# Kernel tuning notes

Hardware: AMD Instinct MI355X
Metric: run time of the kernel (lower is better)

## Reference

```python
import jax, jax.numpy as jnp
import numpy as np

NEG_CAUSAL = -1e10  # matches torch buffer triu(ones*-1e10, diag=1)
NEG_PAD = -10000.0
NUM_HEADS = 16


def setup_inputs() -> dict:
    key = jax.random.key(0)
    ks = jax.random.split(key, 6)
    B, S, D = 2, 2048, 1024
    scale = 0.02
    return {
        "hidden_states": jax.random.normal(ks[0], (B, S, D), jnp.float32),
        "attention_mask": jnp.ones((B, S), jnp.float32),
        "Wq": jax.random.normal(ks[1], (D, D), jnp.float32) * scale,
        "bq": jnp.zeros((D,), jnp.float32),
        "Wk": jax.random.normal(ks[2], (D, D), jnp.float32) * scale,
        "bk": jnp.zeros((D,), jnp.float32),
        "Wv": jax.random.normal(ks[3], (D, D), jnp.float32) * scale,
        "bv": jnp.zeros((D,), jnp.float32),
        "Wo": jax.random.normal(ks[4], (D, D), jnp.float32) * scale,
        "bo": jnp.zeros((D,), jnp.float32),
    }


def reference(hidden_states, attention_mask, Wq, bq, Wk, bk, Wv, bv, Wo, bo):
    B, S, D = hidden_states.shape
    H = NUM_HEADS
    hd = D // H

    def heads(x):  # [B,S,D] -> [B,H,S,hd]
        return x.reshape(B, S, H, hd).transpose(0, 2, 1, 3)

    q = heads(hidden_states @ Wq + bq)
    k = heads(hidden_states @ Wk + bk)
    v = heads(hidden_states @ Wv + bv)

    scores = jnp.einsum("bhqd,bhkd->bhqk", q, k) / jnp.sqrt(jnp.float32(hd))
    causal = jnp.triu(jnp.full((S, S), NEG_CAUSAL, jnp.float32), k=1)
    scores = scores + causal
    # additive padding mask: (1 - m) * -10000, broadcast over heads and query pos
    scores = scores + (1.0 - attention_mask)[:, None, None, :] * NEG_PAD

    probs = jax.nn.softmax(scores, axis=-1)
    # dropout p=0.1 is inactive in eval mode (training=False)
    ctx = jnp.einsum("bhqk,bhkd->bhqd", probs, v)
    ctx = ctx.transpose(0, 2, 1, 3).reshape(B, S, D)
    return ctx @ Wo + bo
```

## Files before the change

### kernel.cpp

```cpp
#include <hip/hip_runtime.h>

typedef __attribute__((ext_vector_type(8))) short short8_t;
typedef __attribute__((ext_vector_type(4))) float float4_t;
typedef unsigned short u16;
typedef unsigned int u32;
typedef unsigned long long u64;

__device__ inline u16 f2bf(float x) {
  union { float f; u32 u; } v; v.f = x;
  u32 r = v.u + 0x7FFFu + ((v.u >> 16) & 1u);
  return (u16)(r >> 16);
}
#if __has_builtin(__builtin_amdgcn_cvt_pk_bf16_f32)
typedef __attribute__((ext_vector_type(2))) __bf16 bf162_t;
__device__ inline u32 pk2(float a, float b) {
  union { bf162_t v; u32 u; } cv;
  cv.v = __builtin_amdgcn_cvt_pk_bf16_f32(a, b);
  return cv.u;
}
#else
__device__ inline u32 pk2(float a, float b) {
  return (u32)f2bf(a) | ((u32)f2bf(b) << 16);
}
#endif

__global__ __launch_bounds__(256) void prologue(const float* __restrict__ X,
                                                const float* __restrict__ Wq, const float* __restrict__ Wk,
                                                const float* __restrict__ Wv, const float* __restrict__ Wo,
                                                u16* __restrict__ Xb, u16* __restrict__ WqkvT,
                                                u16* __restrict__ WoT, const float* __restrict__ maskp,
                                                u32* __restrict__ flags) {
  __shared__ float tls[32][33];
  int bid = blockIdx.x;
  if (bid < 4096) {
    int i = bid * 256 + threadIdx.x;
    float4_t x = ((const float4_t*)X)[i];
    union { u32 u[2]; u64 ll; } o;
    o.u[0] = pk2(x[0], x[1]);
    o.u[1] = pk2(x[2], x[3]);
    ((u64*)Xb)[i] = o.ll;
  } else if (bid < 8192) {
    int t = bid - 4096;
    int mat = t >> 10, tile = t & 1023;
    const float* W = (mat == 0) ? Wq : (mat == 1) ? Wk : (mat == 2) ? Wv : Wo;
    u16* WT = (mat < 3) ? WqkvT + ((size_t)mat << 20) : WoT;
    int tx = threadIdx.x & 31, ty = threadIdx.x >> 5;
    int c0 = (tile & 31) * 32, r0 = (tile >> 5) * 32;
    #pragma unroll
    for (int i = 0; i < 4; ++i)
      tls[ty + i * 8][tx] = W[(r0 + ty + i * 8) * 1024 + c0 + tx];
    __syncthreads();
    #pragma unroll
    for (int i = 0; i < 4; ++i)
      WT[(size_t)(c0 + ty + i * 8) * 1024 + r0 + tx] = f2bf(tls[tx][ty + i * 8]);
  } else {
    int b = bid - 8192;
    const float* mb = maskp + (b << 11) + threadIdx.x * 8;
    bool ok = true;
    #pragma unroll
    for (int i = 0; i < 8; ++i) ok &= (mb[i] == 1.0f);
    u64 bal = __ballot(ok);
    int w = threadIdx.x >> 6;
    if ((threadIdx.x & 63) == 0) tls[0][w] = (bal == ~0ull) ? 1.0f : 0.0f;
    __syncthreads();
    if (threadIdx.x == 0)
      flags[b] = (tls[0][0] != 0.0f && tls[0][1] != 0.0f &&
                  tls[0][2] != 0.0f && tls[0][3] != 0.0f) ? 1u : 0u;
  }
}

__global__ __launch_bounds__(256) void gemm128(const u16* __restrict__ A, const u16* __restrict__ BT,
                                               const float* __restrict__ bias0, const float* __restrict__ bias1,
                                               const float* __restrict__ bias2,
                                               void* __restrict__ o0, void* __restrict__ o1, void* __restrict__ o2,
                                               int mode) {
  __shared__ __align__(16) u16 Als[128 * 64];
  __shared__ __align__(16) u16 Bls[128 * 64];
  int g = blockIdx.x, m0t, n0t;
  if (mode == 4) {
    int mh = g / 384, r = g - mh * 384;
    n0t = r >> 4;
    m0t = mh * 16 + (r & 15);
  } else {
    m0t = g & 31;
    n0t = g >> 5;
  }
  const int m0 = m0t * 128, n0 = n0t * 128;
  const int lane = threadIdx.x & 63, wave = threadIdx.x >> 6;
  const int quad = lane >> 4, c = lane & 15;
  const int wm = wave >> 1, wn = wave & 1;

  const int srow = lane >> 3, schunk = lane & 7;
  int soff[4], dst[4];
  #pragma unroll
  for (int q = 0; q < 4; ++q) {
    int r = wave * 32 + q * 8 + srow;
    soff[q] = r * 1024 + (schunk << 3);
    dst[q]  = r * 64 + ((schunk ^ (r & 7)) << 3);
  }
  const u16* gA = A + (size_t)m0 * 1024;
  const u16* gB = BT + (size_t)n0 * 1024;

  int ar[2][4], br[2][4];
  #pragma unroll
  for (int ko = 0; ko < 2; ++ko) {
    #pragma unroll
    for (int i = 0; i < 4; ++i) {
      int rowa = wm * 64 + i * 16 + c;
      ar[ko][i] = rowa * 64 + (((ko * 4 + quad) ^ (rowa & 7)) << 3);
      int rowb = wn * 64 + i * 16 + c;
      br[ko][i] = rowb * 64 + (((ko * 4 + quad) ^ (rowb & 7)) << 3);
    }
  }

  short8_t ra[4], rb[4];
  #pragma unroll
  for (int q = 0; q < 4; ++q) ra[q] = *(const short8_t*)(gA + soff[q]);
  #pragma unroll
  for (int q = 0; q < 4; ++q) rb[q] = *(const short8_t*)(gB + soff[q]);

  float4_t acc[4][4] = {};
  for (int k0 = 0; k0 < 1024; k0 += 64) {
    #pragma unroll
    for (int q = 0; q < 4; ++q) *(short8_t*)&Als[dst[q]] = ra[q];
    #pragma unroll
    for (int q = 0; q < 4; ++q) *(short8_t*)&Bls[dst[q]] = rb[q];
    __syncthreads();
    if (k0 < 960) {
      #pragma unroll
      for (int q = 0; q < 4; ++q) ra[q] = *(const short8_t*)(gA + soff[q] + k0 + 64);
      #pragma unroll
      for (int q = 0; q < 4; ++q) rb[q] = *(const short8_t*)(gB + soff[q] + k0 + 64);
    }
    #pragma unroll
    for (int ko = 0; ko < 2; ++ko) {
      short8_t af[4], bfr[4];
      #pragma unroll
      for (int i = 0; i < 4; ++i) af[i] = *(const short8_t*)&Als[ar[ko][i]];
      #pragma unroll
      for (int j = 0; j < 4; ++j) bfr[j] = *(const short8_t*)&Bls[br[ko][j]];
      #pragma unroll
      for (int i = 0; i < 4; ++i)
        #pragma unroll
        for (int j = 0; j < 4; ++j)
          acc[i][j] = __builtin_amdgcn_mfma_f32_16x16x32_bf16(af[i], bfr[j], acc[i][j], 0, 0, 0);
    }
    __syncthreads();
  }

  const int mrow = m0 + wm * 64, ncol = n0 + wn * 64;
  if (mode == 3) {
    float* o = (float*)o0;
    #pragma unroll
    for (int i = 0; i < 4; ++i) {
      #pragma unroll
      for (int j = 0; j < 4; ++j) {
        int colb = ncol + j * 16 + c;
        float bv = bias0[colb];
        int rowb = mrow + i * 16 + quad * 4;
        #pragma unroll
        for (int r = 0; r < 4; ++r)
          o[(size_t)(rowb + r) * 1024 + colb] = acc[i][j][r] + bv;
      }
    }
  } else {
    #pragma unroll
    for (int j = 0; j < 4; ++j) {
      int colb = ncol + j * 16 + c;
      int which = colb >> 10;
      int n1 = colb & 1023, h = n1 >> 6, d = n1 & 63;
      const float* bp = (which == 0) ? bias0 : (which == 1 ? bias1 : bias2);
      float bv = bp[n1];
      #pragma unroll
      for (int i = 0; i < 4; ++i) {
        int rowb = mrow + i * 16 + quad * 4;
        int b = rowb >> 11, s = rowb & 2047;
        if (which == 2) {
          u16* o = (u16*)o2 + (((size_t)(b * 16 + h) * 64 + d) * 2048 + s);
          union { u32 u[2]; u64 ll; } ov;
          ov.u[0] = pk2(acc[i][j][0] + bv, acc[i][j][1] + bv);
          ov.u[1] = pk2(acc[i][j][2] + bv, acc[i][j][3] + bv);
          *(u64*)o = ov.ll;
        } else {
          float sc = (which == 0) ? 0.18033688011112042f : 1.0f;
          u16* o = (u16*)((which == 0) ? o0 : o1);
          #pragma unroll
          for (int r = 0; r < 4; ++r)
            o[(((size_t)(b * 16 + h) * 2048 + (s + r)) << 6) + d] = f2bf((acc[i][j][r] + bv) * sc);
        }
      }
    }
  }
}

__device__ inline short8_t p_to_b_swap(const float* p) {
  u32 a0 = pk2(p[0], p[1]), a1 = pk2(p[2], p[3]);
  u32 b0 = pk2(p[4], p[5]), b1 = pk2(p[6], p[7]);
  asm("v_permlane32_swap_b32 %0, %1" : "+v"(a0), "+v"(b0));
  asm("v_permlane32_swap_b32 %0, %1" : "+v"(a1), "+v"(b1));
  asm("v_permlane16_swap_b32 %0, %1" : "+v"(a0), "+v"(b0));
  asm("v_permlane16_swap_b32 %0, %1" : "+v"(a1), "+v"(b1));
  union { u32 u[4]; short8_t v; } pf;
  pf.u[0] = a0; pf.u[1] = a1; pf.u[2] = b0; pf.u[3] = b1;
  return pf.v;
}

__global__ __launch_bounds__(256, 4) void attn_kernel(const u16* __restrict__ Q, const u16* __restrict__ K,
                                                      const u16* __restrict__ VT, const float* __restrict__ mask,
                                                      const u32* __restrict__ flags, u16* __restrict__ ctx) {
  __shared__ __align__(16) u16 Kls[2 * 64 * 64];
  __shared__ __align__(16) u16 Vls[2 * 64 * 64];
  const float C1 = 10000.0f * 1.4426950408889634f;
  int w = threadIdx.x >> 6, lane = threadIdx.x & 63;
  int quad = lane >> 4, c = lane & 15;
  int g = blockIdx.x;
  int bh = (g & 7) * 4 + ((g >> 3) & 3);
  int u = g >> 5;
  int qt = (u < 16) ? (31 - u) : (u - 16);
  int b = bh >> 4, h = bh & 15;
  bool ones = flags && (flags[b] != 0);
  const u16* Kp = K + ((size_t)bh << 17);
  const u16* Vp = VT + ((size_t)bh << 17);
  const float* mp = mask + (b << 11);
  int q0 = qt * 64 + w * 16;

  const u16* Qp = Q + (((size_t)bh * 2048 + q0 + c) << 6) + quad * 8;
  short8_t qf0 = *(const short8_t*)(Qp);
  short8_t qf1 = *(const short8_t*)(Qp + 32);

  const int srow = lane >> 3, schunk = lane & 7;
  const u16* gK[2]; const u16* gV[2]; int dK[2], dV[2];
  #pragma unroll
  for (int i = 0; i < 2; ++i) {
    int R = w * 16 + i * 8 + srow;
    gK[i] = Kp + R * 64 + (schunk << 3);
    dK[i] = R * 64 + ((schunk ^ (R & 7)) << 3);
    gV[i] = Vp + (size_t)R * 2048 + (schunk << 3);
    dV[i] = R * 64 + ((schunk ^ (R & 7)) << 3);
  }

  int koff[4][2];
  #pragma unroll
  for (int kg = 0; kg < 4; ++kg) {
    int r = kg * 16 + c;
    #pragma unroll
    for (int ko = 0; ko < 2; ++ko)
      koff[kg][ko] = r * 64 + (((ko * 4 + quad) ^ (r & 7)) << 3);
  }
  int voff[4][2];
  #pragma unroll
  for (int dblk = 0; dblk < 4; ++dblk) {
    int d = dblk * 16 + c;
    #pragma unroll
    for (int kc = 0; kc < 2; ++kc)
      voff[dblk][kc] = d * 64 + (((kc * 4 + quad) ^ (d & 7)) << 3);
  }

  int ke[8];
  #pragma unroll
  for (int e = 0; e < 8; ++e) ke[e] = ((e >> 2) << 4) + quad * 4 + (e & 3);
  int thr = w * 16 + c;

  float4_t O[4] = {};
  float l = 0.0f;

  short8_t kreg[2], vreg[2];
  #pragma unroll
  for (int i = 0; i < 2; ++i) { kreg[i] = *(const short8_t*)(gK[i]); vreg[i] = *(const short8_t*)(gV[i]); }

  for (int t = 0; t <= qt; ++t) {
    int kb = t << 6;
    int bufo = (t & 1) << 12;
    #pragma unroll
    for (int i = 0; i < 2; ++i) *(short8_t*)&Kls[bufo + dK[i]] = kreg[i];
    #pragma unroll
    for (int i = 0; i < 2; ++i) *(short8_t*)&Vls[bufo + dV[i]] = vreg[i];
    __syncthreads();
    short8_t vf[4][2];
    #pragma unroll
    for (int dblk = 0; dblk < 4; ++dblk)
      #pragma unroll
      for (int kc = 0; kc < 2; ++kc)
        vf[dblk][kc] = *(const short8_t*)&Vls[bufo + voff[dblk][kc]];
    if (t < qt) {
      int kb2 = (t + 1) << 6;
      #pragma unroll
      for (int i = 0; i < 2; ++i) {
        kreg[i] = *(const short8_t*)(gK[i] + (size_t)kb2 * 64);
        vreg[i] = *(const short8_t*)(gV[i] + kb2);
      }
    }
    float4_t s[4];
    __builtin_amdgcn_s_setprio(1);
    #pragma unroll
    for (int kg = 0; kg < 4; ++kg) {
      short8_t k0 = *(const short8_t*)&Kls[bufo + koff[kg][0]];
      short8_t k1 = *(const short8_t*)&Kls[bufo + koff[kg][1]];
      float4_t a = {};
      a = __builtin_amdgcn_mfma_f32_16x16x32_bf16(k0, qf0, a, 0, 0, 0);
      a = __builtin_amdgcn_mfma_f32_16x16x32_bf16(k1, qf1, a, 0, 0, 0);
      s[kg] = a;
    }
    __builtin_amdgcn_s_setprio(0);
    float4_t mpl[4];
    if (!ones) {
      #pragma unroll
      for (int kg = 0; kg < 4; ++kg)
        mpl[kg] = (*(const float4_t*)(mp + kb + kg * 16 + quad * 4) - 1.0f) * C1;
    }
    bool diag = (t == qt);
    short8_t pf[2];
    #pragma unroll
    for (int kc = 0; kc < 2; ++kc) {
      float p[8];
      #pragma unroll
      for (int e = 0; e < 8; ++e) {
        int kg = kc * 2 + (e >> 2);
        p[e] = s[kg][e & 3];
        if (!ones) p[e] += mpl[kg][e & 3];
      }
      if (diag) {
        #pragma unroll
        for (int e = 0; e < 8; ++e) {
          int ko2 = kc * 32 + ke[e];
          p[e] = (ko2 > thr) ? -50.0f : p[e];
        }
      }
      #pragma unroll
      for (int e = 0; e < 8; ++e) p[e] = exp2f(p[e]);
      float t01 = p[0] + p[1], t23 = p[2] + p[3];
      float t45 = p[4] + p[5], t67 = p[6] + p[7];
      l += (t01 + t23) + (t45 + t67);
      pf[kc] = p_to_b_swap(p);
    }
    __builtin_amdgcn_s_setprio(1);
    #pragma unroll
    for (int dblk = 0; dblk < 4; ++dblk) {
      O[dblk] = __builtin_amdgcn_mfma_f32_16x16x32_bf16(vf[dblk][0], pf[0], O[dblk], 0, 0, 0);
      O[dblk] = __builtin_amdgcn_mfma_f32_16x16x32_bf16(vf[dblk][1], pf[1], O[dblk], 0, 0, 0);
    }
    __builtin_amdgcn_s_setprio(0);
  }
  l += __shfl_xor(l, 16);
  l += __shfl_xor(l, 32);
  float rl = 1.0f / l;
  u16* op = ctx + ((size_t)(b * 2048 + q0 + c) * 1024 + h * 64 + quad * 4);
  #pragma unroll
  for (int dblk = 0; dblk < 4; ++dblk) {
    union { u32 uu[2]; u64 ll; } ov;
    ov.uu[0] = pk2(O[dblk][0] * rl, O[dblk][1] * rl);
    ov.uu[1] = pk2(O[dblk][2] * rl, O[dblk][3] * rl);
    *(u64*)(op + dblk * 16) = ov.ll;
  }
}

extern "C" void kernel_launch(void* const* d_in, const int* in_sizes, int n_in,
                              void* d_out, int out_size, void* d_ws, size_t ws_size,
                              hipStream_t stream) {
  const float* X    = (const float*)d_in[0];
  const float* mask = (const float*)d_in[1];
  const float* Wq   = (const float*)d_in[2];
  const float* bq   = (const float*)d_in[3];
  const float* Wk   = (const float*)d_in[4];
  const float* bk   = (const float*)d_in[5];
  const float* Wv   = (const float*)d_in[6];
  const float* bv   = (const float*)d_in[7];
  const float* Wo   = (const float*)d_in[8];
  const float* bo   = (const float*)d_in[9];

  char* w = (char*)d_ws;
  u16* Xb     = (u16*)(w);
  u16* WqkvT  = (u16*)(w + (8ull  << 20));
  u16* WoT    = (u16*)(w + (14ull << 20));
  u16* Qb     = (u16*)(w + (16ull << 20));
  u16* Kb     = (u16*)(w + (24ull << 20));
  u16* VTb    = (u16*)(w + (32ull << 20));
  u16* Ctx    = (u16*)(w + (40ull << 20));
  u32* flags  = (ws_size >= (48ull << 20) + 8) ? (u32*)(w + (48ull << 20)) : nullptr;

  prologue<<<flags ? 8194 : 8192, 256, 0, stream>>>(X, Wq, Wk, Wv, Wo, Xb, WqkvT, WoT, mask, flags);
  gemm128<<<768, 256, 0, stream>>>(Xb, WqkvT, bq, bk, bv, Qb, Kb, VTb, 4);
  attn_kernel<<<1024, 256, 0, stream>>>(Qb, Kb, VTb, mask, flags, Ctx);
  gemm128<<<256, 256, 0, stream>>>(Ctx, WoT, bo, bo, bo, d_out, d_out, d_out, 3);
}
```

Before: 207.5 us.

## Process 128-query tiles per block with two query groups per wave

Each attention block now covers 128 queries (32 per wave, as two 16-row groups), so each K/V tile loaded into shared memory serves twice as many queries and the grid halves to 512 blocks. Row sums are now computed with extra MFMAs against a ones vector instead of scalar adds plus cross-lane shuffles, and V fragments are read from LDS right before use. Causal skipping becomes per-wave (waves skip tiles beyond their rows). The cost is more registers (launch bounds lowered to 2), fewer blocks for load balance, and extra MFMA work for the row sums.

After: 195.4 us. 5.8% less time.

```diff
diff --git a/kernel.cpp b/kernel.cpp
--- a/kernel.cpp
+++ b/kernel.cpp
@@ -205,7 +205,31 @@
   return pf.v;
 }
 
-__global__ __launch_bounds__(256, 4) void attn_kernel(const u16* __restrict__ Q, const u16* __restrict__ K,
+__device__ inline void softmax_half(const float4_t* s, const float4_t* mpl, bool ones,
+                                    bool diag, int thr, int kb, const int* ke, short8_t* pf) {
+  #pragma unroll
+  for (int kc = 0; kc < 2; ++kc) {
+    float p[8];
+    #pragma unroll
+    for (int e = 0; e < 8; ++e) {
+      int kg = kc * 2 + (e >> 2);
+      p[e] = s[kg][e & 3];
+      if (!ones) p[e] += mpl[kg][e & 3];
+    }
+    if (diag) {
+      #pragma unroll
+      for (int e = 0; e < 8; ++e) {
+        int keyg = kb + kc * 32 + ke[e];
+        p[e] = (keyg > thr) ? -50.0f : p[e];
+      }
+    }
+    #pragma unroll
+    for (int e = 0; e < 8; ++e) p[e] = exp2f(p[e]);
+    pf[kc] = p_to_b_swap(p);
+  }
+}
+
+__global__ __launch_bounds__(256, 2) void attn_kernel(const u16* __restrict__ Q, const u16* __restrict__ K,
                                                       const u16* __restrict__ VT, const float* __restrict__ mask,
                                                       const u32* __restrict__ flags, u16* __restrict__ ctx) {
   __shared__ __align__(16) u16 Kls[2 * 64 * 64];
@@ -216,17 +240,20 @@
   int g = blockIdx.x;
   int bh = (g & 7) * 4 + ((g >> 3) & 3);
   int u = g >> 5;
-  int qt = (u < 16) ? (31 - u) : (u - 16);
+  int qt = (u < 8) ? (15 - u) : (u - 8);
   int b = bh >> 4, h = bh & 15;
   bool ones = flags && (flags[b] != 0);
   const u16* Kp = K + ((size_t)bh << 17);
   const u16* Vp = VT + ((size_t)bh << 17);
   const float* mp = mask + (b << 11);
-  int q0 = qt * 64 + w * 16;
+  int q0 = qt * 128 + w * 32;
+  int nt = 2 * qt + 2;
 
   const u16* Qp = Q + (((size_t)bh * 2048 + q0 + c) << 6) + quad * 8;
-  short8_t qf0 = *(const short8_t*)(Qp);
-  short8_t qf1 = *(const short8_t*)(Qp + 32);
+  short8_t qa0 = *(const short8_t*)(Qp);
+  short8_t qa1 = *(const short8_t*)(Qp + 32);
+  short8_t qb0 = *(const short8_t*)(Qp + (16 << 6));
+  short8_t qb1 = *(const short8_t*)(Qp + (16 << 6) + 32);
 
   const int srow = lane >> 3, schunk = lane & 7;
   const u16* gK[2]; const u16* gV[2]; int dK[2], dV[2];
@@ -259,16 +286,19 @@
   int ke[8];
   #pragma unroll
   for (int e = 0; e < 8; ++e) ke[e] = ((e >> 2) << 4) + quad * 4 + (e & 3);
-  int thr = w * 16 + c;
-
-  float4_t O[4] = {};
-  float l = 0.0f;
+  int thrA = q0 + c;
+  int thrB = q0 + 16 + c;
+  union { u32 uu[4]; short8_t v; } onesf;
+  onesf.uu[0] = onesf.uu[1] = onesf.uu[2] = onesf.uu[3] = 0x3F803F80u;
+
+  float4_t OA[4] = {}, OB[4] = {};
+  float4_t lA = {}, lB = {};
 
   short8_t kreg[2], vreg[2];
   #pragma unroll
   for (int i = 0; i < 2; ++i) { kreg[i] = *(const short8_t*)(gK[i]); vreg[i] = *(const short8_t*)(gV[i]); }
 
-  for (int t = 0; t <= qt; ++t) {
+  for (int t = 0; t < nt; ++t) {
     int kb = t << 6;
     int bufo = (t & 1) << 12;
     #pragma unroll
@@ -276,13 +306,7 @@
     #pragma unroll
     for (int i = 0; i < 2; ++i) *(short8_t*)&Vls[bufo + dV[i]] = vreg[i];
     __syncthreads();
-    short8_t vf[4][2];
-    #pragma unroll
-    for (int dblk = 0; dblk < 4; ++dblk)
-      #pragma unroll
-      for (int kc = 0; kc < 2; ++kc)
-        vf[dblk][kc] = *(const short8_t*)&Vls[bufo + voff[dblk][kc]];
-    if (t < qt) {
+    if (t < nt - 1) {
       int kb2 = (t + 1) << 6;
       #pragma unroll
       for (int i = 0; i < 2; ++i) {
@@ -290,16 +314,22 @@
         vreg[i] = *(const short8_t*)(gV[i] + kb2);
       }
     }
-    float4_t s[4];
+    if (kb > q0 + 31) continue;
+
+    float4_t sA[4], sB[4];
     __builtin_amdgcn_s_setprio(1);
     #pragma unroll
     for (int kg = 0; kg < 4; ++kg) {
       short8_t k0 = *(const short8_t*)&Kls[bufo + koff[kg][0]];
       short8_t k1 = *(const short8_t*)&Kls[bufo + koff[kg][1]];
       float4_t a = {};
-      a = __builtin_amdgcn_mfma_f32_16x16x32_bf16(k0, qf0, a, 0, 0, 0);
-      a = __builtin_amdgcn_mfma_f32_16x16x32_bf16(k1, qf1, a, 0, 0, 0);
-      s[kg] = a;
+      a = __builtin_amdgcn_mfma_f32_16x16x32_bf16(k0, qa0, a, 0, 0, 0);
+      a = __builtin_amdgcn_mfma_f32_16x16x32_bf16(k1, qa1, a, 0, 0, 0);
+      sA[kg] = a;
+      float4_t bb = {};
+      bb = __builtin_amdgcn_mfma_f32_16x16x32_bf16(k0, qb0, bb, 0, 0, 0);
+      bb = __builtin_amdgcn_mfma_f32_16x16x32_bf16(k1, qb1, bb, 0, 0, 0);
+      sB[kg] = bb;
     }
     __builtin_amdgcn_s_setprio(0);
     float4_t mpl[4];
@@ -308,49 +338,43 @@
       for (int kg = 0; kg < 4; ++kg)
         mpl[kg] = (*(const float4_t*)(mp + kb + kg * 16 + quad * 4) - 1.0f) * C1;
     }
-    bool diag = (t == qt);
-    short8_t pf[2];
-    #pragma unroll
-    for (int kc = 0; kc < 2; ++kc) {
-      float p[8];
-      #pragma unroll
-      for (int e = 0; e < 8; ++e) {
-        int kg = kc * 2 + (e >> 2);
-        p[e] = s[kg][e & 3];
-        if (!ones) p[e] += mpl[kg][e & 3];
-      }
-      if (diag) {
-        #pragma unroll
-        for (int e = 0; e < 8; ++e) {
-          int ko2 = kc * 32 + ke[e];
-          p[e] = (ko2 > thr) ? -50.0f : p[e];
-        }
-      }
-      #pragma unroll
-      for (int e = 0; e < 8; ++e) p[e] = exp2f(p[e]);
-      float t01 = p[0] + p[1], t23 = p[2] + p[3];
-      float t45 = p[4] + p[5], t67 = p[6] + p[7];
-      l += (t01 + t23) + (t45 + t67);
-      pf[kc] = p_to_b_swap(p);
-    }
+    bool diag = (kb + 63 > q0);
+    short8_t pfA[2], pfB[2];
+    softmax_half(sA, mpl, ones, diag, thrA, kb, ke, pfA);
+    softmax_half(sB, mpl, ones, diag, thrB, kb, ke, pfB);
     __builtin_amdgcn_s_setprio(1);
     #pragma unroll
     for (int dblk = 0; dblk < 4; ++dblk) {
-      O[dblk] = __builtin_amdgcn_mfma_f32_16x16x32_bf16(vf[dblk][0], pf[0], O[dblk], 0, 0, 0);
-      O[dblk] = __builtin_amdgcn_mfma_f32_16x16x32_bf16(vf[dblk][1], pf[1], O[dblk], 0, 0, 0);
-    }
+      short8_t vf0 = *(const short8_t*)&Vls[bufo + voff[dblk][0]];
+      short8_t vf1 = *(const short8_t*)&Vls[bufo + voff[dblk][1]];
+      OA[dblk] = __builtin_amdgcn_mfma_f32_16x16x32_bf16(vf0, pfA[0], OA[dblk], 0, 0, 0);
+      OA[dblk] = __builtin_amdgcn_mfma_f32_16x16x32_bf16(vf1, pfA[1], OA[dblk], 0, 0, 0);
+      OB[dblk] = __builtin_amdgcn_mfma_f32_16x16x32_bf16(vf0, pfB[0], OB[dblk], 0, 0, 0);
+      OB[dblk] = __builtin_amdgcn_mfma_f32_16x16x32_bf16(vf1, pfB[1], OB[dblk], 0, 0, 0);
+    }
+    lA = __builtin_amdgcn_mfma_f32_16x16x32_bf16(onesf.v, pfA[0], lA, 0, 0, 0);
+    lA = __builtin_amdgcn_mfma_f32_16x16x32_bf16(onesf.v, pfA[1], lA, 0, 0, 0);
+    lB = __builtin_amdgcn_mfma_f32_16x16x32_bf16(onesf.v, pfB[0], lB, 0, 0, 0);
+    lB = __builtin_amdgcn_mfma_f32_16x16x32_bf16(onesf.v, pfB[1], lB, 0, 0, 0);
     __builtin_amdgcn_s_setprio(0);
   }
-  l += __shfl_xor(l, 16);
-  l += __shfl_xor(l, 32);
-  float rl = 1.0f / l;
-  u16* op = ctx + ((size_t)(b * 2048 + q0 + c) * 1024 + h * 64 + quad * 4);
+  float rlA = 1.0f / lA[0];
+  u16* opA = ctx + ((size_t)(b * 2048 + q0 + c) * 1024 + h * 64 + quad * 4);
   #pragma unroll
   for (int dblk = 0; dblk < 4; ++dblk) {
     union { u32 uu[2]; u64 ll; } ov;
-    ov.uu[0] = pk2(O[dblk][0] * rl, O[dblk][1] * rl);
-    ov.uu[1] = pk2(O[dblk][2] * rl, O[dblk][3] * rl);
-    *(u64*)(op + dblk * 16) = ov.ll;
+    ov.uu[0] = pk2(OA[dblk][0] * rlA, OA[dblk][1] * rlA);
+    ov.uu[1] = pk2(OA[dblk][2] * rlA, OA[dblk][3] * rlA);
+    *(u64*)(opA + dblk * 16) = ov.ll;
+  }
+  float rlB = 1.0f / lB[0];
+  u16* opB = ctx + ((size_t)(b * 2048 + q0 + 16 + c) * 1024 + h * 64 + quad * 4);
+  #pragma unroll
+  for (int dblk = 0; dblk < 4; ++dblk) {
+    union { u32 uu[2]; u64 ll; } ov;
+    ov.uu[0] = pk2(OB[dblk][0] * rlB, OB[dblk][1] * rlB);
+    ov.uu[1] = pk2(OB[dblk][2] * rlB, OB[dblk][3] * rlB);
+    *(u64*)(opB + dblk * 16) = ov.ll;
   }
 }
 
@@ -380,6 +404,6 @@
 
   prologue<<<flags ? 8194 : 8192, 256, 0, stream>>>(X, Wq, Wk, Wv, Wo, Xb, WqkvT, WoT, mask, flags);
   gemm128<<<768, 256, 0, stream>>>(Xb, WqkvT, bq, bk, bv, Qb, Kb, VTb, 4);
-  attn_kernel<<<1024, 256, 0, stream>>>(Qb, Kb, VTb, mask, flags, Ctx);
+  attn_kernel<<<512, 256, 0, stream>>>(Qb, Kb, VTb, mask, flags, Ctx);
   gemm128<<<256, 256, 0, stream>>>(Ctx, WoT, bo, bo, bo, d_out, d_out, d_out, 3);
 }
```
